# Kernel tuning notes

Hardware: AMD Instinct MI355X
Metric: run time of the kernel (lower is better)

Reference implementation:

```python
import jax, jax.numpy as jnp
import numpy as np

B, N, D = 16, 1024, 768
NEG = -1.0e9

def leaky_relu(x, slope=0.01):
    return jnp.where(x >= 0, x, slope * x)

def setup_inputs() -> dict:
    key = jax.random.key(0)
    ks = jax.random.split(key, 20)
    s = 0.02
    inp = {
        'inputs': jax.random.normal(ks[0], (B, N, D), dtype=jnp.float32),
        'adj_mat': jax.random.randint(ks[1], (B, N, N), 0, 2).astype(jnp.float32),
        # BaseGraphAttNet params
        'W_fc': jax.random.normal(ks[2], (D, D), dtype=jnp.float32) * s,
        'b_fc': jnp.zeros((D,), dtype=jnp.float32),
        'w_q': jax.random.normal(ks[3], (D,), dtype=jnp.float32) * s,
        'b_q': jnp.zeros((), dtype=jnp.float32),
        'w_k': jax.random.normal(ks[4], (D,), dtype=jnp.float32) * s,
        'b_k': jnp.zeros((), dtype=jnp.float32),
        # gating params (6 linears)
        'W_uy': jax.random.normal(ks[5], (D, D), dtype=jnp.float32) * s,
        'b_uy': jnp.zeros((D,), dtype=jnp.float32),
        'W_ux': jax.random.normal(ks[6], (D, D), dtype=jnp.float32) * s,
        'b_ux': jnp.zeros((D,), dtype=jnp.float32),
        'W_ry': jax.random.normal(ks[7], (D, D), dtype=jnp.float32) * s,
        'b_ry': jnp.zeros((D,), dtype=jnp.float32),
        'W_rx': jax.random.normal(ks[8], (D, D), dtype=jnp.float32) * s,
        'b_rx': jnp.zeros((D,), dtype=jnp.float32),
        'W_ty': jax.random.normal(ks[9], (D, D), dtype=jnp.float32) * s,
        'b_ty': jnp.zeros((D,), dtype=jnp.float32),
        'W_tx': jax.random.normal(ks[10], (D, D), dtype=jnp.float32) * s,
        'b_tx': jnp.zeros((D,), dtype=jnp.float32),
    }
    return inp

def reference(inputs, adj_mat, W_fc, b_fc, w_q, b_q, w_k, b_k,
              W_uy, b_uy, W_ux, b_ux, W_ry, b_ry, W_rx, b_rx,
              W_ty, b_ty, W_tx, b_tx):
    # ---- BaseGraphAttNet (residual=False); dropout in eval mode (identity) ----
    feat_proj = jnp.einsum('bnd,ed->bne', inputs, W_fc) + b_fc      # bs x N x D
    q = jnp.einsum('bnd,d->bn', feat_proj, w_q) + b_q               # bs x N
    k = jnp.einsum('bnd,d->bn', feat_proj, w_k) + b_k               # bs x N
    logits = q[:, :, None] + k[:, None, :]                          # bs x N x N
    masked = logits + (1.0 - adj_mat) * NEG
    masked = leaky_relu(masked)
    att = jax.nn.softmax(masked, axis=-1)
    y = jnp.einsum('bnm,bmd->bnd', att, feat_proj)                  # bs x N x D
    # ---- GRU-style gating ----
    u = jax.nn.sigmoid(jnp.einsum('bnd,ed->bne', y, W_uy) + b_uy
                       + jnp.einsum('bnd,ed->bne', inputs, W_ux) + b_ux)
    r = jax.nn.sigmoid(jnp.einsum('bnd,ed->bne', y, W_ry) + b_ry
                       + jnp.einsum('bnd,ed->bne', inputs, W_rx) + b_rx)
    x_tmp = jnp.tanh(jnp.einsum('bnd,ed->bne', y, W_ty) + b_ty
                     + jnp.einsum('bnd,ed->bne', r * inputs, W_tx) + b_tx)
    out = (1.0 - u) * inputs + u * x_tmp
    return out
```

## Files before the change

kernel.cpp:

```cpp
#include <hip/hip_runtime.h>
#include <cmath>

typedef __attribute__((ext_vector_type(8))) short bf16x8;
typedef __attribute__((ext_vector_type(4))) float f32x4;
typedef unsigned short u16;

struct __align__(8) us4 { u16 x, y, z, w; };

__device__ __forceinline__ u16 f2bf(float f) {
    union { float f; unsigned u; } v; v.f = f;
    unsigned u = v.u;
    u += 0x7fffu + ((u >> 16) & 1u);
    return (u16)(u >> 16);
}
__device__ __forceinline__ float bf2f(u16 h) {
    union { unsigned u; float f; } v; v.u = ((unsigned)h) << 16;
    return v.f;
}
__device__ __forceinline__ f32x4 mfma16(bf16x8 a, bf16x8 b, f32x4 c) {
    return __builtin_amdgcn_mfma_f32_16x16x32_bf16(a, b, c, 0, 0, 0);
}
__device__ __forceinline__ void ld_lds16(const u16* g, u16* l) {
    __builtin_amdgcn_global_load_lds(
        (const __attribute__((address_space(1))) unsigned int*)g,
        (__attribute__((address_space(3))) unsigned int*)l, 16, 0, 0);
}

__global__ __launch_bounds__(256) void zqk(float* qv, float* kv) {
    int i = blockIdx.x * 256 + threadIdx.x;
    qv[i] = 0.f; kv[i] = 0.f;
}

__global__ __launch_bounds__(256) void cvtx(const float* __restrict__ in,
                                            u16* __restrict__ Xb, u16* __restrict__ CatA) {
    int i = blockIdx.x * 256 + threadIdx.x;
    float4 f = reinterpret_cast<const float4*>(in)[i];
    us4 o; o.x = f2bf(f.x); o.y = f2bf(f.y); o.z = f2bf(f.z); o.w = f2bf(f.w);
    reinterpret_cast<us4*>(Xb)[i] = o;
    int fe = i * 4, row = fe / 768, col = fe % 768;
    *reinterpret_cast<us4*>(CatA + (size_t)row * 1536 + 768 + col) = o;
}

struct WCvt { const float* s[8]; u16* d[8]; int ld[8]; };
__global__ __launch_bounds__(256) void cvtw(WCvt w) {
    int wi = blockIdx.y;
    int i = blockIdx.x * 256 + threadIdx.x;
    float4 f = reinterpret_cast<const float4*>(w.s[wi])[i];
    us4 o; o.x = f2bf(f.x); o.y = f2bf(f.y); o.z = f2bf(f.z); o.w = f2bf(f.w);
    int fe = i * 4, row = fe / 768, col = fe % 768;
    *reinterpret_cast<us4*>(w.d[wi] + (size_t)row * w.ld[wi] + col) = o;
}

enum { EPI_FPT = 0, EPI_Y, EPI_GATES, EPI_OUT };

struct Epi {
    const float* b_fc; const float* wq; const float* wk; float* qv; float* kv;
    u16* fpT;
    u16* catA;
    const float* b_uy; const float* b_ux; const float* b_ry; const float* b_rx;
    const float* b_ty;
    const u16* xb; u16* ub_o; u16* tyb_o; u16* rxb_o;
    const float* btx; const u16* tyb; const u16* ub; float* of;
};

template<int EPI>
__global__ __launch_bounds__(256) void g128(
    const u16* __restrict__ A, const u16* __restrict__ Bm,
    int K, int ldA, int ldB, size_t zA, size_t zB, Epi e)
{
    __shared__ u16 lA[128 * 32];
    __shared__ u16 lB[128 * 32];

    const int t = threadIdx.x;
    const int w = t >> 6, lane = t & 63, lm = lane & 15, quad = lane >> 4;
    const int row0 = blockIdx.x * 128, col0 = blockIdx.y * 128;

    if constexpr (EPI == EPI_GATES) { if (blockIdx.y >= 12) K = 768; }

    const int rs = t >> 2;
    const int kc = ((t & 3) * 8) ^ ((((rs >> 1) & 3)) << 3);
    u16* dA0 = lA + w * 512;
    u16* dA1 = lA + 2048 + w * 512;
    u16* dB0 = lB + w * 512;
    u16* dB1 = lB + 2048 + w * 512;

    const u16* As = A + (size_t)blockIdx.z * zA;
    const u16* Bs = Bm + (size_t)blockIdx.z * zB;
    const u16* gA0 = As + (size_t)(row0 + rs) * ldA + kc;
    const u16* gA1 = As + (size_t)(row0 + 64 + rs) * ldA + kc;
    const u16* gB0 = Bs + (size_t)(col0 + rs) * ldB + kc;
    const u16* gB1 = Bs + (size_t)(col0 + 64 + rs) * ldB + kc;

    const int rw0 = (w & 1) * 64, cw0 = (w >> 1) * 64;
    const int sw = (lm >> 1) & 3;
    const u16* la[4]; const u16* lb[4];
#pragma unroll
    for (int i = 0; i < 4; i++) la[i] = lA + (rw0 + i * 16 + lm) * 32 + ((quad ^ sw) * 8);
#pragma unroll
    for (int j = 0; j < 4; j++) lb[j] = lB + (cw0 + j * 16 + lm) * 32 + ((quad ^ sw) * 8);

    f32x4 acc[4][4] = {};

    for (int k0 = 0; k0 < K; k0 += 32) {
        if (k0 != 0) __syncthreads();
        ld_lds16(gA0 + k0, dA0);
        ld_lds16(gA1 + k0, dA1);
        ld_lds16(gB0 + k0, dB0);
        ld_lds16(gB1 + k0, dB1);
        __syncthreads();

        bf16x8 a[4], b[4];
#pragma unroll
        for (int i = 0; i < 4; i++) a[i] = *reinterpret_cast<const bf16x8*>(la[i]);
#pragma unroll
        for (int j = 0; j < 4; j++) b[j] = *reinterpret_cast<const bf16x8*>(lb[j]);
#pragma unroll
        for (int i = 0; i < 4; i++)
#pragma unroll
            for (int j = 0; j < 4; j++)
                acc[i][j] = mfma16(a[i], b[j], acc[i][j]);
    }

#pragma unroll
    for (int i = 0; i < 4; i++) {
        const int gr = row0 + rw0 + i * 16 + quad * 4;
        if constexpr (EPI == EPI_FPT) {
            float qp[4] = {}, kp[4] = {};
            int bb = gr >> 10, nn = gr & 1023;
#pragma unroll
            for (int j = 0; j < 4; j++) {
                int gc = col0 + cw0 + j * 16 + lm;
                float bias = e.b_fc[gc];
                float v0 = acc[i][j][0] + bias, v1 = acc[i][j][1] + bias;
                float v2 = acc[i][j][2] + bias, v3 = acc[i][j][3] + bias;
                us4 o; o.x = f2bf(v0); o.y = f2bf(v1); o.z = f2bf(v2); o.w = f2bf(v3);
                *reinterpret_cast<us4*>(e.fpT + (size_t)bb * 786432 + (size_t)gc * 1024 + nn) = o;
                float wqv = e.wq[gc], wkv = e.wk[gc];
                qp[0] = fmaf(v0, wqv, qp[0]); qp[1] = fmaf(v1, wqv, qp[1]);
                qp[2] = fmaf(v2, wqv, qp[2]); qp[3] = fmaf(v3, wqv, qp[3]);
                kp[0] = fmaf(v0, wkv, kp[0]); kp[1] = fmaf(v1, wkv, kp[1]);
                kp[2] = fmaf(v2, wkv, kp[2]); kp[3] = fmaf(v3, wkv, kp[3]);
            }
#pragma unroll
            for (int r = 0; r < 4; r++) {
                float q = qp[r], k = kp[r];
#pragma unroll
                for (int m = 1; m < 16; m <<= 1) { q += __shfl_xor(q, m); k += __shfl_xor(k, m); }
                if (lm == 0) { atomicAdd(e.qv + gr + r, q); atomicAdd(e.kv + gr + r, k); }
            }
        } else if constexpr (EPI == EPI_Y) {
            size_t grow = (size_t)blockIdx.z * 1024 + gr;
#pragma unroll
            for (int j = 0; j < 4; j++) {
                int gc = col0 + cw0 + j * 16 + lm;
#pragma unroll
                for (int r = 0; r < 4; r++)
                    e.catA[(grow + r) * 1536 + gc] = f2bf(acc[i][j][r]);
            }
        } else if constexpr (EPI == EPI_GATES) {
            int grp = blockIdx.y / 6;
            int oc0 = (blockIdx.y % 6) * 128 + cw0;
#pragma unroll
            for (int j = 0; j < 4; j++) {
                int gc = oc0 + j * 16 + lm;
                if (grp == 0) {
                    float bias = e.b_uy[gc] + e.b_ux[gc];
#pragma unroll
                    for (int r = 0; r < 4; r++) {
                        size_t idx = (size_t)(gr + r) * 768 + gc;
                        e.ub_o[idx] = f2bf(1.f / (1.f + __expf(-(acc[i][j][r] + bias))));
                    }
                } else if (grp == 1) {
                    float bias = e.b_ry[gc] + e.b_rx[gc];
#pragma unroll
                    for (int r = 0; r < 4; r++) {
                        size_t idx = (size_t)(gr + r) * 768 + gc;
                        float rr = 1.f / (1.f + __expf(-(acc[i][j][r] + bias)));
                        e.rxb_o[idx] = f2bf(rr * bf2f(e.xb[idx]));
                    }
                } else {
                    float bias = e.b_ty[gc];
#pragma unroll
                    for (int r = 0; r < 4; r++) {
                        size_t idx = (size_t)(gr + r) * 768 + gc;
                        e.tyb_o[idx] = f2bf(acc[i][j][r] + bias);
                    }
                }
            }
        } else {
#pragma unroll
            for (int j = 0; j < 4; j++) {
                int gc = col0 + cw0 + j * 16 + lm;
                float bias = e.btx[gc];
#pragma unroll
                for (int r = 0; r < 4; r++) {
                    size_t idx = (size_t)(gr + r) * 768 + gc;
                    float tt = tanhf(acc[i][j][r] + bias + bf2f(e.tyb[idx]));
                    float uu = bf2f(e.ub[idx]);
                    float xv = bf2f(e.xb[idx]);
                    e.of[idx] = (1.f - uu) * xv + uu * tt;
                }
            }
        }
    }
}

__global__ __launch_bounds__(256) void k_soft(const float* __restrict__ adj,
                                              const float* __restrict__ qv,
                                              const float* __restrict__ kv,
                                              const float* __restrict__ bq,
                                              const float* __restrict__ bk,
                                              u16* __restrict__ attb) {
    int bn = blockIdx.x;
    int b = bn >> 10;
    const float* adjrow = adj + (size_t)bn * 1024;
    const float* krow = kv + (b << 10);
    float q = qv[bn] + bq[0] + bk[0];
    int m0 = threadIdx.x * 4;

    float4 a4 = *reinterpret_cast<const float4*>(adjrow + m0);
    float4 k4 = *reinterpret_cast<const float4*>(krow + m0);
    float v[4];
    v[0] = q + k4.x + (1.f - a4.x) * -1.0e9f;
    v[1] = q + k4.y + (1.f - a4.y) * -1.0e9f;
    v[2] = q + k4.z + (1.f - a4.z) * -1.0e9f;
    v[3] = q + k4.w + (1.f - a4.w) * -1.0e9f;
#pragma unroll
    for (int t = 0; t < 4; t++) v[t] = v[t] >= 0.f ? v[t] : 0.01f * v[t];

    float mx = fmaxf(fmaxf(v[0], v[1]), fmaxf(v[2], v[3]));
    __shared__ float red[4];
#pragma unroll
    for (int off = 32; off; off >>= 1) mx = fmaxf(mx, __shfl_xor(mx, off));
    if ((threadIdx.x & 63) == 0) red[threadIdx.x >> 6] = mx;
    __syncthreads();
    mx = fmaxf(fmaxf(red[0], red[1]), fmaxf(red[2], red[3]));

    float s = 0.f;
#pragma unroll
    for (int t = 0; t < 4; t++) { v[t] = __expf(v[t] - mx); s += v[t]; }
#pragma unroll
    for (int off = 32; off; off >>= 1) s += __shfl_xor(s, off);
    __syncthreads();
    if ((threadIdx.x & 63) == 0) red[threadIdx.x >> 6] = s;
    __syncthreads();
    s = red[0] + red[1] + red[2] + red[3];
    float inv = 1.f / s;

    us4 o;
    o.x = f2bf(v[0] * inv); o.y = f2bf(v[1] * inv);
    o.z = f2bf(v[2] * inv); o.w = f2bf(v[3] * inv);
    *reinterpret_cast<us4*>(attb + (size_t)bn * 1024 + m0) = o;
}

extern "C" void kernel_launch(void* const* d_in, const int* in_sizes, int n_in,
                              void* d_out, int out_size, void* d_ws, size_t ws_size,
                              hipStream_t stream) {
    const float* x    = (const float*)d_in[0];
    const float* adj  = (const float*)d_in[1];
    const float* W_fc = (const float*)d_in[2];
    const float* b_fc = (const float*)d_in[3];
    const float* w_q  = (const float*)d_in[4];
    const float* b_q  = (const float*)d_in[5];
    const float* w_k  = (const float*)d_in[6];
    const float* b_k  = (const float*)d_in[7];
    const float* W_uy = (const float*)d_in[8];
    const float* b_uy = (const float*)d_in[9];
    const float* W_ux = (const float*)d_in[10];
    const float* b_ux = (const float*)d_in[11];
    const float* W_ry = (const float*)d_in[12];
    const float* b_ry = (const float*)d_in[13];
    const float* W_rx = (const float*)d_in[14];
    const float* b_rx = (const float*)d_in[15];
    const float* W_ty = (const float*)d_in[16];
    const float* b_ty = (const float*)d_in[17];
    const float* W_tx = (const float*)d_in[18];
    const float* b_tx = (const float*)d_in[19];

    char* ws = (char*)d_ws;
    u16*   Xb    = (u16*)  (ws + 0);
    u16*   Wfc_b = (u16*)  (ws + 25165824);
    u16*   Wtx_b = (u16*)  (ws + 26345472);
    u16*   Wg    = (u16*)  (ws + 27525120);
    u16*   fpT   = (u16*)  (ws + 34603008);
    float* qv    = (float*)(ws + 59768832);
    float* kv    = (float*)(ws + 59834368);
    u16*   attb  = (u16*)  (ws + 59899904);
    u16*   u_b   = (u16*)  (ws + 59899904);
    u16*   CatA  = (u16*)  (ws + 93454336);
    u16*   ty_b  = (u16*)  (ws + 143785984);
    u16*   rxb   = (u16*)  (ws + 168951808);

    zqk<<<64, 256, 0, stream>>>(qv, kv);
    cvtx<<<12288, 256, 0, stream>>>(x, Xb, CatA);

    WCvt wc;
    wc.s[0] = W_fc; wc.d[0] = Wfc_b;            wc.ld[0] = 768;
    wc.s[1] = W_tx; wc.d[1] = Wtx_b;            wc.ld[1] = 768;
    wc.s[2] = W_uy; wc.d[2] = Wg;               wc.ld[2] = 1536;
    wc.s[3] = W_ux; wc.d[3] = Wg + 768;         wc.ld[3] = 1536;
    wc.s[4] = W_ry; wc.d[4] = Wg + 768*1536;    wc.ld[4] = 1536;
    wc.s[5] = W_rx; wc.d[5] = Wg + 768*1536+768;wc.ld[5] = 1536;
    wc.s[6] = W_ty; wc.d[6] = Wg + 1536*1536;   wc.ld[6] = 1536;
    wc.s[7] = W_ty; wc.d[7] = Wg + 1536*1536+768; wc.ld[7] = 1536;
    cvtw<<<dim3(576, 8), 256, 0, stream>>>(wc);

    Epi e{};
    e = Epi{}; e.b_fc = b_fc; e.wq = w_q; e.wk = w_k; e.qv = qv; e.kv = kv; e.fpT = fpT;
    g128<EPI_FPT><<<dim3(128, 6), 256, 0, stream>>>(Xb, Wfc_b, 768, 768, 768, 0, 0, e);

    k_soft<<<16384, 256, 0, stream>>>(adj, qv, kv, b_q, b_k, attb);

    e = Epi{}; e.catA = CatA;
    g128<EPI_Y><<<dim3(8, 6, 16), 256, 0, stream>>>(attb, fpT, 1024, 1024, 1024,
                                                    1048576, 786432, e);
    e = Epi{}; e.b_uy = b_uy; e.b_ux = b_ux; e.b_ry = b_ry; e.b_rx = b_rx; e.b_ty = b_ty;
    e.xb = Xb; e.ub_o = u_b; e.tyb_o = ty_b; e.rxb_o = rxb;
    g128<EPI_GATES><<<dim3(128, 18), 256, 0, stream>>>(CatA, Wg, 1536, 1536, 1536, 0, 0, e);

    e = Epi{}; e.btx = b_tx; e.tyb = ty_b; e.ub = u_b; e.xb = Xb; e.of = (float*)d_out;
    g128<EPI_OUT><<<dim3(128, 6), 256, 0, stream>>>(rxb, Wtx_b, 768, 768, 768, 0, 0, e);
}
```

Before: 475.7 us.

## Fuse y·W_ty into output GEMM, drop Xb copy, one-wave-per-row softmax

The y·W_ty product moves out of the gates GEMM into the final GEMM as a second K phase (y·W_ty + (r*x)·W_tx), which removes the ty_b intermediate round trip and shrinks the gates grid from 18 to 12 column groups. The separate bf16 copy of the input is dropped, with x read from the second half of CatA instead, and zeroing of q/k is folded into the conversion kernel, removing one launch. Softmax now uses one wavefront per row, which avoids block-level LDS reductions and barriers. The trade-off is a longer K loop in the output GEMM and strided reads of x.

```diff
diff --git a/kernel.cpp b/kernel.cpp
--- a/kernel.cpp
+++ b/kernel.cpp
@@ -26,70 +26,61 @@
         (__attribute__((address_space(3))) unsigned int*)l, 16, 0, 0);
 }
 
-__global__ __launch_bounds__(256) void zqk(float* qv, float* kv) {
-    int i = blockIdx.x * 256 + threadIdx.x;
-    qv[i] = 0.f; kv[i] = 0.f;
-}
-
 __global__ __launch_bounds__(256) void cvtx(const float* __restrict__ in,
-                                            u16* __restrict__ Xb, u16* __restrict__ CatA) {
+                                            u16* __restrict__ CatA, float* __restrict__ qkz) {
     int i = blockIdx.x * 256 + threadIdx.x;
     float4 f = reinterpret_cast<const float4*>(in)[i];
     us4 o; o.x = f2bf(f.x); o.y = f2bf(f.y); o.z = f2bf(f.z); o.w = f2bf(f.w);
-    reinterpret_cast<us4*>(Xb)[i] = o;
-    int fe = i * 4, row = fe / 768, col = fe % 768;
+    int row = i / 192, col = (i % 192) * 4;
     *reinterpret_cast<us4*>(CatA + (size_t)row * 1536 + 768 + col) = o;
-}
-
-struct WCvt { const float* s[8]; u16* d[8]; int ld[8]; };
+    if (i < 8192) reinterpret_cast<float4*>(qkz)[i] = float4{0.f, 0.f, 0.f, 0.f};
+}
+
+struct WCvt { const float* s[7]; u16* d[7]; int ld[7]; };
 __global__ __launch_bounds__(256) void cvtw(WCvt w) {
     int wi = blockIdx.y;
     int i = blockIdx.x * 256 + threadIdx.x;
     float4 f = reinterpret_cast<const float4*>(w.s[wi])[i];
     us4 o; o.x = f2bf(f.x); o.y = f2bf(f.y); o.z = f2bf(f.z); o.w = f2bf(f.w);
-    int fe = i * 4, row = fe / 768, col = fe % 768;
+    int row = i / 192, col = (i % 192) * 4;
     *reinterpret_cast<us4*>(w.d[wi] + (size_t)row * w.ld[wi] + col) = o;
 }
 
 enum { EPI_FPT = 0, EPI_Y, EPI_GATES, EPI_OUT };
 
 struct Epi {
-    const float* b_fc; const float* wq; const float* wk; float* qv; float* kv;
+    const float* b1; const float* b2; const float* b3; const float* b4;
+    const float* wq; const float* wk; float* qv; float* kv;
     u16* fpT;
     u16* catA;
-    const float* b_uy; const float* b_ux; const float* b_ry; const float* b_rx;
-    const float* b_ty;
-    const u16* xb; u16* ub_o; u16* tyb_o; u16* rxb_o;
-    const float* btx; const u16* tyb; const u16* ub; float* of;
+    const u16* xb;
+    u16* ub_o; u16* rxb_o;
+    const u16* ub; float* of;
 };
 
-template<int EPI>
+template<int EPI, int PH>
 __global__ __launch_bounds__(256) void g128(
-    const u16* __restrict__ A, const u16* __restrict__ Bm,
-    int K, int ldA, int ldB, size_t zA, size_t zB, Epi e)
+    const u16* __restrict__ A1, const u16* __restrict__ B1,
+    const u16* __restrict__ A2, const u16* __restrict__ B2,
+    int K, int ldA1, int ldB1, int ldA2, int ldB2,
+    size_t zA, size_t zB, Epi e)
 {
     __shared__ u16 lA[128 * 32];
     __shared__ u16 lB[128 * 32];
 
     const int t = threadIdx.x;
     const int w = t >> 6, lane = t & 63, lm = lane & 15, quad = lane >> 4;
-    const int row0 = blockIdx.x * 128, col0 = blockIdx.y * 128;
-
-    if constexpr (EPI == EPI_GATES) { if (blockIdx.y >= 12) K = 768; }
+    const int row0 = blockIdx.x * 128;
+    int col0, grp = 0;
+    if constexpr (EPI == EPI_GATES) { grp = blockIdx.y / 6; col0 = (blockIdx.y % 6) * 128; }
+    else col0 = blockIdx.y * 128;
 
     const int rs = t >> 2;
     const int kc = ((t & 3) * 8) ^ ((((rs >> 1) & 3)) << 3);
     u16* dA0 = lA + w * 512;
-    u16* dA1 = lA + 2048 + w * 512;
+    u16* dA1p = lA + 2048 + w * 512;
     u16* dB0 = lB + w * 512;
-    u16* dB1 = lB + 2048 + w * 512;
-
-    const u16* As = A + (size_t)blockIdx.z * zA;
-    const u16* Bs = Bm + (size_t)blockIdx.z * zB;
-    const u16* gA0 = As + (size_t)(row0 + rs) * ldA + kc;
-    const u16* gA1 = As + (size_t)(row0 + 64 + rs) * ldA + kc;
-    const u16* gB0 = Bs + (size_t)(col0 + rs) * ldB + kc;
-    const u16* gB1 = Bs + (size_t)(col0 + 64 + rs) * ldB + kc;
+    u16* dB1p = lB + 2048 + w * 512;
 
     const int rw0 = (w & 1) * 64, cw0 = (w >> 1) * 64;
     const int sw = (lm >> 1) & 3;
@@ -100,25 +91,39 @@
     for (int j = 0; j < 4; j++) lb[j] = lB + (cw0 + j * 16 + lm) * 32 + ((quad ^ sw) * 8);
 
     f32x4 acc[4][4] = {};
-
-    for (int k0 = 0; k0 < K; k0 += 32) {
-        if (k0 != 0) __syncthreads();
-        ld_lds16(gA0 + k0, dA0);
-        ld_lds16(gA1 + k0, dA1);
-        ld_lds16(gB0 + k0, dB0);
-        ld_lds16(gB1 + k0, dB1);
-        __syncthreads();
-
-        bf16x8 a[4], b[4];
-#pragma unroll
-        for (int i = 0; i < 4; i++) a[i] = *reinterpret_cast<const bf16x8*>(la[i]);
-#pragma unroll
-        for (int j = 0; j < 4; j++) b[j] = *reinterpret_cast<const bf16x8*>(lb[j]);
-#pragma unroll
-        for (int i = 0; i < 4; i++)
-#pragma unroll
-            for (int j = 0; j < 4; j++)
-                acc[i][j] = mfma16(a[i], b[j], acc[i][j]);
+    bool first = true;
+
+#pragma unroll
+    for (int ph = 0; ph < PH; ph++) {
+        const u16* As; const u16* Bs; int ldA, ldB;
+        if (ph == 0) { As = A1 + (size_t)blockIdx.z * zA; Bs = B1 + (size_t)blockIdx.z * zB; ldA = ldA1; ldB = ldB1; }
+        else         { As = A2; Bs = B2; ldA = ldA2; ldB = ldB2; }
+        if constexpr (EPI == EPI_GATES) Bs += (size_t)grp * (768 * 1536);
+        const u16* gA0 = As + (size_t)(row0 + rs) * ldA + kc;
+        const u16* gA1 = As + (size_t)(row0 + 64 + rs) * ldA + kc;
+        const u16* gB0 = Bs + (size_t)(col0 + rs) * ldB + kc;
+        const u16* gB1 = Bs + (size_t)(col0 + 64 + rs) * ldB + kc;
+
+        for (int k0 = 0; k0 < K; k0 += 32) {
+            if (!first) __syncthreads();
+            first = false;
+            ld_lds16(gA0 + k0, dA0);
+            ld_lds16(gA1 + k0, dA1p);
+            ld_lds16(gB0 + k0, dB0);
+            ld_lds16(gB1 + k0, dB1p);
+            __syncthreads();
+
+            bf16x8 a[4], b[4];
+#pragma unroll
+            for (int i = 0; i < 4; i++) a[i] = *reinterpret_cast<const bf16x8*>(la[i]);
+#pragma unroll
+            for (int j = 0; j < 4; j++) b[j] = *reinterpret_cast<const bf16x8*>(lb[j]);
+#pragma unroll
+            for (int i = 0; i < 4; i++)
+#pragma unroll
+                for (int j = 0; j < 4; j++)
+                    acc[i][j] = mfma16(a[i], b[j], acc[i][j]);
+        }
     }
 
 #pragma unroll
@@ -130,7 +135,7 @@
 #pragma unroll
             for (int j = 0; j < 4; j++) {
                 int gc = col0 + cw0 + j * 16 + lm;
-                float bias = e.b_fc[gc];
+                float bias = e.b1[gc];
                 float v0 = acc[i][j][0] + bias, v1 = acc[i][j][1] + bias;
                 float v2 = acc[i][j][2] + bias, v3 = acc[i][j][3] + bias;
                 us4 o; o.x = f2bf(v0); o.y = f2bf(v1); o.z = f2bf(v2); o.w = f2bf(v3);
@@ -158,32 +163,24 @@
                     e.catA[(grow + r) * 1536 + gc] = f2bf(acc[i][j][r]);
             }
         } else if constexpr (EPI == EPI_GATES) {
-            int grp = blockIdx.y / 6;
-            int oc0 = (blockIdx.y % 6) * 128 + cw0;
 #pragma unroll
             for (int j = 0; j < 4; j++) {
-                int gc = oc0 + j * 16 + lm;
+                int gc = col0 + cw0 + j * 16 + lm;
                 if (grp == 0) {
-                    float bias = e.b_uy[gc] + e.b_ux[gc];
+                    float bias = e.b1[gc] + e.b2[gc];
 #pragma unroll
                     for (int r = 0; r < 4; r++) {
                         size_t idx = (size_t)(gr + r) * 768 + gc;
                         e.ub_o[idx] = f2bf(1.f / (1.f + __expf(-(acc[i][j][r] + bias))));
                     }
-                } else if (grp == 1) {
-                    float bias = e.b_ry[gc] + e.b_rx[gc];
+                } else {
+                    float bias = e.b3[gc] + e.b4[gc];
 #pragma unroll
                     for (int r = 0; r < 4; r++) {
                         size_t idx = (size_t)(gr + r) * 768 + gc;
                         float rr = 1.f / (1.f + __expf(-(acc[i][j][r] + bias)));
-                        e.rxb_o[idx] = f2bf(rr * bf2f(e.xb[idx]));
-                    }
-                } else {
-                    float bias = e.b_ty[gc];
-#pragma unroll
-                    for (int r = 0; r < 4; r++) {
-                        size_t idx = (size_t)(gr + r) * 768 + gc;
-                        e.tyb_o[idx] = f2bf(acc[i][j][r] + bias);
+                        float xv = bf2f(e.xb[(size_t)(gr + r) * 1536 + gc]);
+                        e.rxb_o[idx] = f2bf(rr * xv);
                     }
                 }
             }
@@ -191,13 +188,13 @@
 #pragma unroll
             for (int j = 0; j < 4; j++) {
                 int gc = col0 + cw0 + j * 16 + lm;
-                float bias = e.btx[gc];
+                float bias = e.b1[gc] + e.b2[gc];
 #pragma unroll
                 for (int r = 0; r < 4; r++) {
                     size_t idx = (size_t)(gr + r) * 768 + gc;
-                    float tt = tanhf(acc[i][j][r] + bias + bf2f(e.tyb[idx]));
+                    float tt = tanhf(acc[i][j][r] + bias);
                     float uu = bf2f(e.ub[idx]);
-                    float xv = bf2f(e.xb[idx]);
+                    float xv = bf2f(e.xb[(size_t)(gr + r) * 1536 + gc]);
                     e.of[idx] = (1.f - uu) * xv + uu * tt;
                 }
             }
@@ -205,52 +202,54 @@
     }
 }
 
-__global__ __launch_bounds__(256) void k_soft(const float* __restrict__ adj,
-                                              const float* __restrict__ qv,
-                                              const float* __restrict__ kv,
-                                              const float* __restrict__ bq,
-                                              const float* __restrict__ bk,
-                                              u16* __restrict__ attb) {
-    int bn = blockIdx.x;
+__global__ __launch_bounds__(256) void k_soft4(const float* __restrict__ adj,
+                                               const float* __restrict__ qv,
+                                               const float* __restrict__ kv,
+                                               const float* __restrict__ bq,
+                                               const float* __restrict__ bk,
+                                               u16* __restrict__ attb) {
+    int wv = threadIdx.x >> 6, lane = threadIdx.x & 63;
+    int bn = blockIdx.x * 4 + wv;
     int b = bn >> 10;
-    const float* adjrow = adj + (size_t)bn * 1024;
-    const float* krow = kv + (b << 10);
+    const float* adjrow = adj + (size_t)bn * 1024 + lane * 16;
+    const float* krow = kv + (b << 10) + lane * 16;
     float q = qv[bn] + bq[0] + bk[0];
-    int m0 = threadIdx.x * 4;
-
-    float4 a4 = *reinterpret_cast<const float4*>(adjrow + m0);
-    float4 k4 = *reinterpret_cast<const float4*>(krow + m0);
-    float v[4];
-    v[0] = q + k4.x + (1.f - a4.x) * -1.0e9f;
-    v[1] = q + k4.y + (1.f - a4.y) * -1.0e9f;
-    v[2] = q + k4.z + (1.f - a4.z) * -1.0e9f;
-    v[3] = q + k4.w + (1.f - a4.w) * -1.0e9f;
-#pragma unroll
-    for (int t = 0; t < 4; t++) v[t] = v[t] >= 0.f ? v[t] : 0.01f * v[t];
-
-    float mx = fmaxf(fmaxf(v[0], v[1]), fmaxf(v[2], v[3]));
-    __shared__ float red[4];
+
+    float v[16];
+#pragma unroll
+    for (int c = 0; c < 4; c++) {
+        float4 a4 = *reinterpret_cast<const float4*>(adjrow + c * 4);
+        float4 k4 = *reinterpret_cast<const float4*>(krow + c * 4);
+        float* vv = v + c * 4;
+        vv[0] = q + k4.x + (1.f - a4.x) * -1.0e9f;
+        vv[1] = q + k4.y + (1.f - a4.y) * -1.0e9f;
+        vv[2] = q + k4.z + (1.f - a4.z) * -1.0e9f;
+        vv[3] = q + k4.w + (1.f - a4.w) * -1.0e9f;
+    }
+#pragma unroll
+    for (int t = 0; t < 16; t++) v[t] = v[t] >= 0.f ? v[t] : 0.01f * v[t];
+
+    float mx = v[0];
+#pragma unroll
+    for (int t = 1; t < 16; t++) mx = fmaxf(mx, v[t]);
 #pragma unroll
     for (int off = 32; off; off >>= 1) mx = fmaxf(mx, __shfl_xor(mx, off));
-    if ((threadIdx.x & 63) == 0) red[threadIdx.x >> 6] = mx;
-    __syncthreads();
-    mx = fmaxf(fmaxf(red[0], red[1]), fmaxf(red[2], red[3]));
 
     float s = 0.f;
 #pragma unroll
-    for (int t = 0; t < 4; t++) { v[t] = __expf(v[t] - mx); s += v[t]; }
+    for (int t = 0; t < 16; t++) { v[t] = __expf(v[t] - mx); s += v[t]; }
 #pragma unroll
     for (int off = 32; off; off >>= 1) s += __shfl_xor(s, off);
-    __syncthreads();
-    if ((threadIdx.x & 63) == 0) red[threadIdx.x >> 6] = s;
-    __syncthreads();
-    s = red[0] + red[1] + red[2] + red[3];
     float inv = 1.f / s;
 
-    us4 o;
-    o.x = f2bf(v[0] * inv); o.y = f2bf(v[1] * inv);
-    o.z = f2bf(v[2] * inv); o.w = f2bf(v[3] * inv);
-    *reinterpret_cast<us4*>(attb + (size_t)bn * 1024 + m0) = o;
+    u16* orow = attb + (size_t)bn * 1024 + lane * 16;
+#pragma unroll
+    for (int c = 0; c < 4; c++) {
+        us4 o;
+        o.x = f2bf(v[c * 4 + 0] * inv); o.y = f2bf(v[c * 4 + 1] * inv);
+        o.z = f2bf(v[c * 4 + 2] * inv); o.w = f2bf(v[c * 4 + 3] * inv);
+        *reinterpret_cast<us4*>(orow + c * 4) = o;
+    }
 }
 
 extern "C" void kernel_launch(void* const* d_in, const int* in_sizes, int n_in,
@@ -278,46 +277,46 @@
     const float* b_tx = (const float*)d_in[19];
 
     char* ws = (char*)d_ws;
-    u16*   Xb    = (u16*)  (ws + 0);
-    u16*   Wfc_b = (u16*)  (ws + 25165824);
-    u16*   Wtx_b = (u16*)  (ws + 26345472);
-    u16*   Wg    = (u16*)  (ws + 27525120);
-    u16*   fpT   = (u16*)  (ws + 34603008);
-    float* qv    = (float*)(ws + 59768832);
-    float* kv    = (float*)(ws + 59834368);
-    u16*   attb  = (u16*)  (ws + 59899904);
-    u16*   u_b   = (u16*)  (ws + 59899904);
-    u16*   CatA  = (u16*)  (ws + 93454336);
-    u16*   ty_b  = (u16*)  (ws + 143785984);
-    u16*   rxb   = (u16*)  (ws + 168951808);
-
-    zqk<<<64, 256, 0, stream>>>(qv, kv);
-    cvtx<<<12288, 256, 0, stream>>>(x, Xb, CatA);
+    u16*   CatA  = (u16*)  (ws + 0);
+    u16*   Wfc_b = (u16*)  (ws + 50331648);
+    u16*   Wty_b = (u16*)  (ws + 51511296);
+    u16*   Wtx_b = (u16*)  (ws + 52690944);
+    u16*   Wg    = (u16*)  (ws + 53870592);
+    u16*   fpT   = (u16*)  (ws + 58589184);
+    float* qv    = (float*)(ws + 83755008);
+    float* kv    = (float*)(ws + 83820544);
+    u16*   attb  = (u16*)  (ws + 83886080);
+    u16*   u_b   = (u16*)  (ws + 83886080);
+    u16*   rxb   = (u16*)  (ws + 117440512);
+
+    cvtx<<<12288, 256, 0, stream>>>(x, CatA, qv);
 
     WCvt wc;
-    wc.s[0] = W_fc; wc.d[0] = Wfc_b;            wc.ld[0] = 768;
-    wc.s[1] = W_tx; wc.d[1] = Wtx_b;            wc.ld[1] = 768;
-    wc.s[2] = W_uy; wc.d[2] = Wg;               wc.ld[2] = 1536;
-    wc.s[3] = W_ux; wc.d[3] = Wg + 768;         wc.ld[3] = 1536;
-    wc.s[4] = W_ry; wc.d[4] = Wg + 768*1536;    wc.ld[4] = 1536;
-    wc.s[5] = W_rx; wc.d[5] = Wg + 768*1536+768;wc.ld[5] = 1536;
-    wc.s[6] = W_ty; wc.d[6] = Wg + 1536*1536;   wc.ld[6] = 1536;
-    wc.s[7] = W_ty; wc.d[7] = Wg + 1536*1536+768; wc.ld[7] = 1536;
-    cvtw<<<dim3(576, 8), 256, 0, stream>>>(wc);
+    wc.s[0] = W_fc; wc.d[0] = Wfc_b;              wc.ld[0] = 768;
+    wc.s[1] = W_ty; wc.d[1] = Wty_b;              wc.ld[1] = 768;
+    wc.s[2] = W_tx; wc.d[2] = Wtx_b;              wc.ld[2] = 768;
+    wc.s[3] = W_uy; wc.d[3] = Wg;                 wc.ld[3] = 1536;
+    wc.s[4] = W_ux; wc.d[4] = Wg + 768;           wc.ld[4] = 1536;
+    wc.s[5] = W_ry; wc.d[5] = Wg + 768 * 1536;    wc.ld[5] = 1536;
+    wc.s[6] = W_rx; wc.d[6] = Wg + 768 * 1536 + 768; wc.ld[6] = 1536;
+    cvtw<<<dim3(576, 7), 256, 0, stream>>>(wc);
 
     Epi e{};
-    e = Epi{}; e.b_fc = b_fc; e.wq = w_q; e.wk = w_k; e.qv = qv; e.kv = kv; e.fpT = fpT;
-    g128<EPI_FPT><<<dim3(128, 6), 256, 0, stream>>>(Xb, Wfc_b, 768, 768, 768, 0, 0, e);
-
-    k_soft<<<16384, 256, 0, stream>>>(adj, qv, kv, b_q, b_k, attb);
+    e = Epi{}; e.b1 = b_fc; e.wq = w_q; e.wk = w_k; e.qv = qv; e.kv = kv; e.fpT = fpT;
+    g128<EPI_FPT, 1><<<dim3(128, 6), 256, 0, stream>>>(CatA + 768, Wfc_b, nullptr, nullptr,
+                                                       768, 1536, 768, 0, 0, 0, 0, e);
+
+    k_soft4<<<4096, 256, 0, stream>>>(adj, qv, kv, b_q, b_k, attb);
 
     e = Epi{}; e.catA = CatA;
-    g128<EPI_Y><<<dim3(8, 6, 16), 256, 0, stream>>>(attb, fpT, 1024, 1024, 1024,
-                                                    1048576, 786432, e);
-    e = Epi{}; e.b_uy = b_uy; e.b_ux = b_ux; e.b_ry = b_ry; e.b_rx = b_rx; e.b_ty = b_ty;
-    e.xb = Xb; e.ub_o = u_b; e.tyb_o = ty_b; e.rxb_o = rxb;
-    g128<EPI_GATES><<<dim3(128, 18), 256, 0, stream>>>(CatA, Wg, 1536, 1536, 1536, 0, 0, e);
-
-    e = Epi{}; e.btx = b_tx; e.tyb = ty_b; e.ub = u_b; e.xb = Xb; e.of = (float*)d_out;
-    g128<EPI_OUT><<<dim3(128, 6), 256, 0, stream>>>(rxb, Wtx_b, 768, 768, 768, 0, 0, e);
-}
+    g128<EPI_Y, 1><<<dim3(8, 6, 16), 256, 0, stream>>>(attb, fpT, nullptr, nullptr,
+                                                       1024, 1024, 1024, 0, 0,
+                                                       1048576, 786432, e);
+    e = Epi{}; e.b1 = b_uy; e.b2 = b_ux; e.b3 = b_ry; e.b4 = b_rx;
+    e.xb = CatA + 768; e.ub_o = u_b; e.rxb_o = rxb;
+    g128<EPI_GATES, 1><<<dim3(128, 12), 256, 0, stream>>>(CatA, Wg, nullptr, nullptr,
+                                                          1536, 1536, 1536, 0, 0, 0, 0, e);
+    e = Epi{}; e.b1 = b_ty; e.b2 = b_tx; e.ub = u_b; e.xb = CatA + 768; e.of = (float*)d_out;
+    g128<EPI_OUT, 2><<<dim3(128, 6), 256, 0, stream>>>(CatA, Wty_b, rxb, Wtx_b,
+                                                       768, 1536, 768, 768, 768, 0, 0, e);
+}
```

Result: faster. 462.8 us (-2.7%).
